# Optimization experiments

Measured on AMD Instinct MI355X. Metric: run time of the kernel, lower is better.

Reference implementation:

```python
import jax, jax.numpy as jnp
import numpy as np

N, E, D, H, C, HID, ED = 50000, 800000, 128, 8, 16, 512, 32


def setup_inputs() -> dict:
    key = jax.random.key(0)
    ks = jax.random.split(key, 16)
    s = 0.05
    return {
        "h": jax.random.normal(ks[0], (N, D), jnp.float32),
        "edge_index": jax.random.randint(ks[1], (2, E), 0, N, jnp.int64),
        "edge_attr": jax.random.normal(ks[2], (E, ED), jnp.float32),
        "w1": jax.random.normal(ks[3], (D, HID), jnp.float32) * s,
        "b1": jnp.zeros((HID,), jnp.float32),
        "w2": jax.random.normal(ks[4], (HID, D), jnp.float32) * s,
        "b2": jnp.zeros((D,), jnp.float32),
        "ln_g": jnp.ones((D,), jnp.float32),
        "ln_b": jnp.zeros((D,), jnp.float32),
        "Wl": jax.random.normal(ks[5], (D, H * C), jnp.float32) * s,
        "bl": jnp.zeros((H * C,), jnp.float32),
        "Wr": jax.random.normal(ks[6], (D, H * C), jnp.float32) * s,
        "br": jnp.zeros((H * C,), jnp.float32),
        "We": jax.random.normal(ks[7], (ED, H * C), jnp.float32) * s,
        "att": jax.random.normal(ks[8], (H, C), jnp.float32) * s,
        "bias_out": jnp.zeros((H * C,), jnp.float32),
    }


def _layer_norm(x, g, b, eps=1e-5):
    mu = jnp.mean(x, axis=-1, keepdims=True)
    var = jnp.var(x, axis=-1, keepdims=True)
    return (x - mu) * jax.lax.rsqrt(var + eps) * g + b


def reference(h, edge_index, edge_attr, w1, b1, w2, b2, ln_g, ln_b,
              Wl, bl, Wr, br, We, att, bias_out):
    # FFN + residual + LayerNorm (dropout = identity in eval)
    u = jax.nn.relu(h @ w1 + b1) @ w2 + b2
    v = _layer_norm(h + u, ln_g, ln_b)

    src, dst = edge_index[0], edge_index[1]
    # GATv2Conv: separate source/target transforms + edge transform
    xl = (v @ Wl + bl).reshape(N, H, C)
    xr = (v @ Wr + br).reshape(N, H, C)
    xe = (edge_attr @ We).reshape(E, H, C)
    x = jax.nn.leaky_relu(xl[src] + xr[dst] + xe, 0.2)  # [E,H,C]
    logits = jnp.einsum("ehc,hc->eh", x, att)            # [E,H]
    # segment softmax over incoming edges of each destination node
    m = jax.lax.stop_gradient(jax.ops.segment_max(logits, dst, num_segments=N))
    ex = jnp.exp(logits - m[dst])
    den = jax.ops.segment_sum(ex, dst, num_segments=N)
    alpha = ex / den[dst]                                # [E,H]
    msg = xl[src] * alpha[..., None]                     # [E,H,C]
    w = jax.ops.segment_sum(msg, dst, num_segments=N).reshape(N, H * C) + bias_out
    output = _layer_norm(w + v, ln_g, ln_b)
    return output, alpha
```

## Files before the change

### kernel.cpp

```cpp
#include <hip/hip_runtime.h>
#include <math.h>

#define N_NODES 50000
#define E_EDGES 800000
#define D_DIM   128
#define H_HEADS 8
#define C_CH    16
#define HID_DIM 512
#define ED_DIM  32

typedef __attribute__((ext_vector_type(8))) short short8;
typedef __attribute__((ext_vector_type(4))) float f32x4;

__device__ __forceinline__ short f2bf(float f) {
    unsigned u = __float_as_uint(f);
    return (short)((u + 0x7FFFu + ((u >> 16) & 1u)) >> 16);
}
__device__ __forceinline__ float bf2f(short s) {
    return __uint_as_float(((unsigned)(unsigned short)s) << 16);
}

__global__ __launch_bounds__(64) void repack_kernel(
    const float* __restrict__ w1, const float* __restrict__ w2,
    const float* __restrict__ Wl, const float* __restrict__ Wr,
    const float* __restrict__ We,
    short8* __restrict__ w1p, short8* __restrict__ w2p,
    short8* __restrict__ Wlp, short8* __restrict__ Wrp,
    short8* __restrict__ Wep)
{
    int b = blockIdx.x;
    const float* src; short8* dst; int Nw, nc, rel;
    if (b < 128)      { src = w1; dst = w1p; Nw = 512; nc = 4;  rel = b; }
    else if (b < 256) { src = w2; dst = w2p; Nw = 128; nc = 16; rel = b - 128; }
    else if (b < 288) { src = Wl; dst = Wlp; Nw = 128; nc = 4;  rel = b - 256; }
    else if (b < 320) { src = Wr; dst = Wrp; Nw = 128; nc = 4;  rel = b - 288; }
    else              { src = We; dst = Wep; Nw = 128; nc = 1;  rel = b - 320; }
    int t = rel / nc, c = rel % nc;
    int l = threadIdx.x, quad = l >> 4, col = l & 15;
    short8 r;
    #pragma unroll
    for (int j = 0; j < 8; ++j)
        r[j] = f2bf(src[(size_t)(c * 32 + quad * 8 + j) * Nw + t * 16 + col]);
    dst[(size_t)rel * 64 + l] = r;
}

__global__ __launch_bounds__(256) void count_kernel(
    const int* __restrict__ edge_index, unsigned* __restrict__ cnt,
    unsigned short* __restrict__ rank)
{
    int e = blockIdx.x * 256 + threadIdx.x;
    int dst = edge_index[E_EDGES + e];
    rank[e] = (unsigned short)atomicAdd(&cnt[dst], 1u);
}

__global__ __launch_bounds__(256) void node_ffn_mfma(
    const float* __restrict__ h,
    const float* __restrict__ b1, const float* __restrict__ b2,
    const float* __restrict__ ln_g, const float* __restrict__ ln_b,
    const float* __restrict__ bl, const float* __restrict__ br,
    const short8* __restrict__ w1p, const short8* __restrict__ w2p,
    const short8* __restrict__ Wlp, const short8* __restrict__ Wrp,
    float* __restrict__ v_out, float* __restrict__ xl_out, float* __restrict__ xr_out)
{
    __shared__ short hid_bf[16 * 520];
    __shared__ float v_s[16 * 132];
    __shared__ short v_bf[16 * 136];

    const int tid = threadIdx.x;
    const int w = tid >> 6, lane = tid & 63;
    const int m = lane & 15, quad = lane >> 4;
    const int n0 = blockIdx.x * 16;

    short8 af[4];
    #pragma unroll
    for (int c = 0; c < 4; ++c) {
        const float* hp = h + (size_t)(n0 + m) * 128 + c * 32 + quad * 8;
        float4 p0 = ((const float4*)hp)[0];
        float4 p1 = ((const float4*)hp)[1];
        short8 a;
        a[0] = f2bf(p0.x); a[1] = f2bf(p0.y); a[2] = f2bf(p0.z); a[3] = f2bf(p0.w);
        a[4] = f2bf(p1.x); a[5] = f2bf(p1.y); a[6] = f2bf(p1.z); a[7] = f2bf(p1.w);
        af[c] = a;
    }

    {
        f32x4 acc[8];
        #pragma unroll
        for (int t = 0; t < 8; ++t) acc[t] = (f32x4){0.f, 0.f, 0.f, 0.f};
        #pragma unroll
        for (int t = 0; t < 8; ++t) {
            int tile = w * 8 + t;
            #pragma unroll
            for (int c = 0; c < 4; ++c) {
                short8 bf = w1p[(size_t)(tile * 4 + c) * 64 + lane];
                acc[t] = __builtin_amdgcn_mfma_f32_16x16x32_bf16(af[c], bf, acc[t], 0, 0, 0);
            }
        }
        #pragma unroll
        for (int t = 0; t < 8; ++t) {
            int col = (w * 8 + t) * 16 + m;
            float bias = b1[col];
            #pragma unroll
            for (int r = 0; r < 4; ++r) {
                int row = quad * 4 + r;
                hid_bf[row * 520 + col] = f2bf(fmaxf(acc[t][r] + bias, 0.f));
            }
        }
    }
    __syncthreads();

    {
        f32x4 acc2[2];
        acc2[0] = (f32x4){0.f, 0.f, 0.f, 0.f};
        acc2[1] = (f32x4){0.f, 0.f, 0.f, 0.f};
        #pragma unroll 4
        for (int c = 0; c < 16; ++c) {
            short8 a = *(const short8*)&hid_bf[m * 520 + c * 32 + quad * 8];
            #pragma unroll
            for (int t = 0; t < 2; ++t) {
                short8 bf = w2p[(size_t)((w * 2 + t) * 16 + c) * 64 + lane];
                acc2[t] = __builtin_amdgcn_mfma_f32_16x16x32_bf16(a, bf, acc2[t], 0, 0, 0);
            }
        }
        #pragma unroll
        for (int t = 0; t < 2; ++t) {
            int col = (w * 2 + t) * 16 + m;
            float bias = b2[col];
            #pragma unroll
            for (int r = 0; r < 4; ++r) {
                int row = quad * 4 + r;
                v_s[row * 132 + col] = acc2[t][r] + bias + h[(size_t)(n0 + row) * 128 + col];
            }
        }
    }
    __syncthreads();

    {
        float g0 = ln_g[lane], g1 = ln_g[lane + 64];
        float be0 = ln_b[lane], be1 = ln_b[lane + 64];
        #pragma unroll
        for (int p = 0; p < 4; ++p) {
            int nd = w * 4 + p;
            float x0 = v_s[nd * 132 + lane], x1 = v_s[nd * 132 + lane + 64];
            float s = x0 + x1, ss = x0 * x0 + x1 * x1;
            #pragma unroll
            for (int off = 1; off < 64; off <<= 1) {
                s  += __shfl_xor(s, off);
                ss += __shfl_xor(ss, off);
            }
            float mu = s * (1.f / 128.f);
            float var = ss * (1.f / 128.f) - mu * mu;
            float rs = rsqrtf(var + 1e-5f);
            float y0 = (x0 - mu) * rs * g0 + be0;
            float y1 = (x1 - mu) * rs * g1 + be1;
            v_out[(size_t)(n0 + nd) * 128 + lane]      = y0;
            v_out[(size_t)(n0 + nd) * 128 + lane + 64] = y1;
            v_bf[nd * 136 + lane]      = f2bf(y0);
            v_bf[nd * 136 + lane + 64] = f2bf(y1);
        }
    }
    __syncthreads();

    {
        short8 af3[4];
        #pragma unroll
        for (int c = 0; c < 4; ++c)
            af3[c] = *(const short8*)&v_bf[m * 136 + c * 32 + quad * 8];
        f32x4 accl[2], accr[2];
        #pragma unroll
        for (int t = 0; t < 2; ++t) {
            accl[t] = (f32x4){0.f, 0.f, 0.f, 0.f};
            accr[t] = (f32x4){0.f, 0.f, 0.f, 0.f};
        }
        #pragma unroll
        for (int t = 0; t < 2; ++t) {
            int tile = w * 2 + t;
            #pragma unroll
            for (int c = 0; c < 4; ++c) {
                accl[t] = __builtin_amdgcn_mfma_f32_16x16x32_bf16(
                    af3[c], Wlp[(size_t)(tile * 4 + c) * 64 + lane], accl[t], 0, 0, 0);
                accr[t] = __builtin_amdgcn_mfma_f32_16x16x32_bf16(
                    af3[c], Wrp[(size_t)(tile * 4 + c) * 64 + lane], accr[t], 0, 0, 0);
            }
        }
        #pragma unroll
        for (int t = 0; t < 2; ++t) {
            int col = (w * 2 + t) * 16 + m;
            float bld = bl[col], brd = br[col];
            #pragma unroll
            for (int r = 0; r < 4; ++r) {
                int row = quad * 4 + r;
                xl_out[(size_t)(n0 + row) * 128 + col] = accl[t][r] + bld;
                xr_out[(size_t)(n0 + row) * 128 + col] = accr[t][r] + brd;
            }
        }
    }
}

__global__ __launch_bounds__(1024) void scan_kernel(
    const unsigned* __restrict__ cnt, int* __restrict__ rowstart)
{
    __shared__ int wsum[16];
    __shared__ int s_carry;
    const int t = threadIdx.x, wv = t >> 6, lane = t & 63;
    if (t == 0) s_carry = 0;
    __syncthreads();
    for (int b4 = 0; b4 < N_NODES / 4; b4 += 1024) {
        int i4 = b4 + t;
        int4 v4 = make_int4(0, 0, 0, 0);
        if (i4 < N_NODES / 4) v4 = ((const int4*)cnt)[i4];
        int v = v4.x + v4.y + v4.z + v4.w;
        int s = v;
        #pragma unroll
        for (int off = 1; off < 64; off <<= 1) {
            int nb = __shfl_up(s, off);
            if (lane >= off) s += nb;
        }
        if (lane == 63) wsum[wv] = s;
        __syncthreads();
        int woff = s_carry;
        for (int k = 0; k < wv; ++k) woff += wsum[k];
        int tot = woff + s;
        if (i4 < N_NODES / 4) {
            int e0 = woff + s - v;
            int4 r;
            r.x = e0;
            r.y = e0 + v4.x;
            r.z = r.y + v4.y;
            r.w = r.z + v4.z;
            ((int4*)rowstart)[i4] = r;
        }
        __syncthreads();
        if (t == 1023) s_carry = tot;
    }
}

__global__ __launch_bounds__(256) void scatter_kernel(
    const int* __restrict__ edge_index, const unsigned short* __restrict__ rank,
    const int* __restrict__ rowstart, int* __restrict__ eidx,
    unsigned* __restrict__ srcdst)
{
    int e = blockIdx.x * 256 + threadIdx.x;
    if (e >= E_EDGES) return;
    int src = edge_index[e];
    int dst = edge_index[E_EDGES + e];
    int pos = rowstart[dst] + (int)rank[e];
    eidx[pos] = e;
    srcdst[pos] = (unsigned)src | ((unsigned)dst << 16);
}

__global__ __launch_bounds__(256) void edge_logits_mfma(
    const int* __restrict__ eidx, const unsigned* __restrict__ srcdst,
    const float* __restrict__ edge_attr,
    const short8* __restrict__ Wep, const float* __restrict__ att,
    const float* __restrict__ xl, const float* __restrict__ xr,
    float* __restrict__ logits_out)
{
    __shared__ short8 We_f[512];
    __shared__ short xe_s[64 * 136];
    __shared__ int e_s[64];
    __shared__ unsigned sd_s[64];
    const int tid = threadIdx.x;
    const int w = tid >> 6, lane = tid & 63;
    const int m = lane & 15, quad = lane >> 4;
    const int p0b = blockIdx.x * 64;

    We_f[tid]       = Wep[tid];
    We_f[tid + 256] = Wep[tid + 256];
    if (tid < 64) {
        int pos = p0b + tid;
        e_s[tid]  = eidx[pos];
        sd_s[tid] = srcdst[pos];
    }
    __syncthreads();

    const float* eap = edge_attr + (size_t)e_s[w * 16 + m] * 32 + quad * 8;
    float4 p0 = ((const float4*)eap)[0];
    float4 p1 = ((const float4*)eap)[1];
    short8 a;
    a[0] = f2bf(p0.x); a[1] = f2bf(p0.y); a[2] = f2bf(p0.z); a[3] = f2bf(p0.w);
    a[4] = f2bf(p1.x); a[5] = f2bf(p1.y); a[6] = f2bf(p1.z); a[7] = f2bf(p1.w);

    f32x4 acc[8];
    #pragma unroll
    for (int t = 0; t < 8; ++t) acc[t] = (f32x4){0.f, 0.f, 0.f, 0.f};
    #pragma unroll
    for (int t = 0; t < 8; ++t)
        acc[t] = __builtin_amdgcn_mfma_f32_16x16x32_bf16(a, We_f[t * 64 + lane], acc[t], 0, 0, 0);

    #pragma unroll
    for (int t = 0; t < 8; ++t) {
        #pragma unroll
        for (int r = 0; r < 4; ++r)
            xe_s[(w * 16 + quad * 4 + r) * 136 + t * 16 + m] = f2bf(acc[t][r]);
    }
    __syncthreads();

    const int g = quad;
    const int s = m;
    const int d0 = s * 8;
    float4 at0 = ((const float4*)(att + d0))[0];
    float4 at1 = ((const float4*)(att + d0))[1];

    #pragma unroll
    for (int p = 0; p < 4; ++p) {
        int el = p * 16 + w * 4 + g;
        unsigned sd = sd_s[el];
        int src = (int)(sd & 0xffffu);
        int dst = (int)(sd >> 16);
        const float4* xlp = (const float4*)(xl + (size_t)src * 128 + d0);
        const float4* xrp = (const float4*)(xr + (size_t)dst * 128 + d0);
        float4 a0 = xlp[0], a1 = xlp[1];
        float4 r0 = xrp[0], r1 = xrp[1];
        short8 xe8 = *(const short8*)&xe_s[el * 136 + d0];

        float xv[8] = { a0.x + r0.x + bf2f(xe8[0]), a0.y + r0.y + bf2f(xe8[1]),
                        a0.z + r0.z + bf2f(xe8[2]), a0.w + r0.w + bf2f(xe8[3]),
                        a1.x + r1.x + bf2f(xe8[4]), a1.y + r1.y + bf2f(xe8[5]),
                        a1.z + r1.z + bf2f(xe8[6]), a1.w + r1.w + bf2f(xe8[7]) };
        float atv[8] = { at0.x, at0.y, at0.z, at0.w, at1.x, at1.y, at1.z, at1.w };
        float pq = 0.f;
        #pragma unroll
        for (int dd = 0; dd < 8; ++dd) {
            float x = xv[dd];
            x = (x > 0.f) ? x : 0.2f * x;
            pq += x * atv[dd];
        }
        pq += __shfl_xor(pq, 1);
        if ((s & 1) == 0) {
            int e = e_s[el];
            logits_out[(size_t)e * 8 + (s >> 1)] = pq;
        }
    }
}

__global__ __launch_bounds__(256) void node_aggregate_kernel(
    const int* __restrict__ eidx, const int* __restrict__ rowstart,
    const unsigned* __restrict__ cnt, const unsigned* __restrict__ srcdst,
    const float* __restrict__ xl, const float* __restrict__ v,
    const float* __restrict__ bias_out,
    const float* __restrict__ ln_g, const float* __restrict__ ln_b,
    float* __restrict__ alphabuf, float* __restrict__ out)
{
    const int wv = threadIdx.x >> 6, lane = threadIdx.x & 63;
    const int n = blockIdx.x * 4 + wv;
    if (n >= N_NODES) return;
    const int start = rowstart[n];
    const int num = (int)cnt[n];

    const int hh = lane & 7;
    const int slot = lane >> 3;

    float den = 0.f;
    for (int i = slot; i < num; i += 8) {
        int e = eidx[start + i];
        den += expf(alphabuf[(size_t)e * 8 + hh]);
    }
    den += __shfl_xor(den, 8);
    den += __shfl_xor(den, 16);
    den += __shfl_xor(den, 32);
    float inv = 1.f / den;

    const int g = lane >> 4, s = lane & 15;
    const int h3 = s >> 1;
    float iv3 = __shfl(inv, h3);
    float acc[8] = {0.f, 0.f, 0.f, 0.f, 0.f, 0.f, 0.f, 0.f};
    for (int i = 0; i < num; i += 4) {
        int ii = i + g;
        if (ii < num) {
            int e = eidx[start + ii];
            int src = (int)(srcdst[start + ii] & 0xffffu);
            float lg = alphabuf[(size_t)e * 8 + h3];
            float al = expf(lg) * iv3;
            if ((s & 1) == 0) alphabuf[(size_t)e * 8 + h3] = al;
            const float4* xp = (const float4*)(xl + (size_t)src * 128 + s * 8);
            float4 q0 = xp[0], q1 = xp[1];
            acc[0] += q0.x * al; acc[1] += q0.y * al;
            acc[2] += q0.z * al; acc[3] += q0.w * al;
            acc[4] += q1.x * al; acc[5] += q1.y * al;
            acc[6] += q1.z * al; acc[7] += q1.w * al;
        }
    }
    #pragma unroll
    for (int k = 0; k < 8; ++k) {
        acc[k] += __shfl_xor(acc[k], 16);
        acc[k] += __shfl_xor(acc[k], 32);
    }

    const float* vp = v + (size_t)n * 128 + s * 8;
    float4 v0 = ((const float4*)vp)[0], v1 = ((const float4*)vp)[1];
    float4 b0 = ((const float4*)(bias_out + s * 8))[0];
    float4 b1 = ((const float4*)(bias_out + s * 8))[1];
    float x[8];
    x[0] = acc[0] + b0.x + v0.x; x[1] = acc[1] + b0.y + v0.y;
    x[2] = acc[2] + b0.z + v0.z; x[3] = acc[3] + b0.w + v0.w;
    x[4] = acc[4] + b1.x + v1.x; x[5] = acc[5] + b1.y + v1.y;
    x[6] = acc[6] + b1.z + v1.z; x[7] = acc[7] + b1.w + v1.w;
    float sm = 0.f, ssm = 0.f;
    #pragma unroll
    for (int k = 0; k < 8; ++k) { sm += x[k]; ssm += x[k] * x[k]; }
    #pragma unroll
    for (int off = 1; off < 16; off <<= 1) {
        sm  += __shfl_xor(sm, off);
        ssm += __shfl_xor(ssm, off);
    }
    float mu = sm * (1.f / 128.f);
    float var = ssm * (1.f / 128.f) - mu * mu;
    float rs = rsqrtf(var + 1e-5f);
    if (g == 0) {
        float4 g0 = ((const float4*)(ln_g + s * 8))[0];
        float4 g1 = ((const float4*)(ln_g + s * 8))[1];
        float4 be0 = ((const float4*)(ln_b + s * 8))[0];
        float4 be1 = ((const float4*)(ln_b + s * 8))[1];
        float4 o0, o1;
        o0.x = (x[0] - mu) * rs * g0.x + be0.x;
        o0.y = (x[1] - mu) * rs * g0.y + be0.y;
        o0.z = (x[2] - mu) * rs * g0.z + be0.z;
        o0.w = (x[3] - mu) * rs * g0.w + be0.w;
        o1.x = (x[4] - mu) * rs * g1.x + be1.x;
        o1.y = (x[5] - mu) * rs * g1.y + be1.y;
        o1.z = (x[6] - mu) * rs * g1.z + be1.z;
        o1.w = (x[7] - mu) * rs * g1.w + be1.w;
        float4* op = (float4*)(out + (size_t)n * 128 + s * 8);
        op[0] = o0; op[1] = o1;
    }
}

extern "C" void kernel_launch(void* const* d_in, const int* in_sizes, int n_in,
                              void* d_out, int out_size, void* d_ws, size_t ws_size,
                              hipStream_t stream)
{
    const float* h        = (const float*)d_in[0];
    const int*   edge_idx = (const int*)  d_in[1];
    const float* edge_attr= (const float*)d_in[2];
    const float* w1       = (const float*)d_in[3];
    const float* b1       = (const float*)d_in[4];
    const float* w2       = (const float*)d_in[5];
    const float* b2       = (const float*)d_in[6];
    const float* ln_g     = (const float*)d_in[7];
    const float* ln_b     = (const float*)d_in[8];
    const float* Wl       = (const float*)d_in[9];
    const float* bl       = (const float*)d_in[10];
    const float* Wr       = (const float*)d_in[11];
    const float* br       = (const float*)d_in[12];
    const float* We       = (const float*)d_in[13];
    const float* att      = (const float*)d_in[14];
    const float* bias_out = (const float*)d_in[15];

    float* out   = (float*)d_out;
    float* alpha = out + (size_t)N_NODES * 128;

    short8* w1p = (short8*)alpha;
    short8* w2p = w1p + 128 * 64;
    short8* Wlp = w2p + 128 * 64;
    short8* Wrp = Wlp + 32 * 64;

    float*          v        = (float*)d_ws;
    float*          xl       = v  + (size_t)N_NODES * 128;
    float*          xr       = xl + (size_t)N_NODES * 128;
    unsigned*       cnt      = (unsigned*)(xr + (size_t)N_NODES * 128);
    int*            rowstart = (int*)(cnt + N_NODES);
    unsigned short* rank     = (unsigned short*)(rowstart + N_NODES);
    short8*         Wep      = (short8*)(rank + E_EDGES);
    int*            eidx     = (int*)(Wep + 512);
    unsigned*       srcdst   = (unsigned*)(eidx + E_EDGES);

    hipMemsetAsync(cnt, 0, (size_t)N_NODES * sizeof(unsigned), stream);

    repack_kernel<<<328, 64, 0, stream>>>(w1, w2, Wl, Wr, We,
                                          w1p, w2p, Wlp, Wrp, Wep);
    count_kernel<<<E_EDGES / 256, 256, 0, stream>>>(edge_idx, cnt, rank);
    node_ffn_mfma<<<N_NODES / 16, 256, 0, stream>>>(
        h, b1, b2, ln_g, ln_b, bl, br, w1p, w2p, Wlp, Wrp, v, xl, xr);
    scan_kernel<<<1, 1024, 0, stream>>>(cnt, rowstart);
    scatter_kernel<<<(E_EDGES + 255) / 256, 256, 0, stream>>>(
        edge_idx, rank, rowstart, eidx, srcdst);
    edge_logits_mfma<<<E_EDGES / 64, 256, 0, stream>>>(
        eidx, srcdst, edge_attr, Wep, att, xl, xr, alpha);
    node_aggregate_kernel<<<(N_NODES + 3) / 4, 256, 0, stream>>>(
        eidx, rowstart, cnt, srcdst, xl, v, bias_out, ln_g, ln_b, alpha, out);
}
```

Before: 496.6 us.

## Store xl/xr in bf16 and keep logits in CSR order

The node FFN kernel now writes the xl and xr projections as bf16 instead of fp32. This halves the bytes of the random per-edge gathers in the logits and aggregation kernels. Logits are also written to a CSR-ordered scratch buffer, so the aggregation kernel reads them contiguously instead of through the eidx indirection; only the final alpha is scattered to edge order. The cost is extra bf16 rounding on xl/xr, which affects accuracy, and a separate E×8 logits buffer in the workspace.

```diff
diff --git a/kernel.cpp b/kernel.cpp
--- a/kernel.cpp
+++ b/kernel.cpp
@@ -60,7 +60,8 @@
     const float* __restrict__ bl, const float* __restrict__ br,
     const short8* __restrict__ w1p, const short8* __restrict__ w2p,
     const short8* __restrict__ Wlp, const short8* __restrict__ Wrp,
-    float* __restrict__ v_out, float* __restrict__ xl_out, float* __restrict__ xr_out)
+    float* __restrict__ v_out,
+    unsigned short* __restrict__ xl_bf_out, unsigned short* __restrict__ xr_bf_out)
 {
     __shared__ short hid_bf[16 * 520];
     __shared__ float v_s[16 * 132];
@@ -190,8 +191,8 @@
             #pragma unroll
             for (int r = 0; r < 4; ++r) {
                 int row = quad * 4 + r;
-                xl_out[(size_t)(n0 + row) * 128 + col] = accl[t][r] + bld;
-                xr_out[(size_t)(n0 + row) * 128 + col] = accr[t][r] + brd;
+                xl_bf_out[(size_t)(n0 + row) * 128 + col] = (unsigned short)f2bf(accl[t][r] + bld);
+                xr_bf_out[(size_t)(n0 + row) * 128 + col] = (unsigned short)f2bf(accr[t][r] + brd);
             }
         }
     }
@@ -253,8 +254,8 @@
     const int* __restrict__ eidx, const unsigned* __restrict__ srcdst,
     const float* __restrict__ edge_attr,
     const short8* __restrict__ Wep, const float* __restrict__ att,
-    const float* __restrict__ xl, const float* __restrict__ xr,
-    float* __restrict__ logits_out)
+    const unsigned short* __restrict__ xl_bf, const unsigned short* __restrict__ xr_bf,
+    float* __restrict__ logits_csr)
 {
     __shared__ short8 We_f[512];
     __shared__ short xe_s[64 * 136];
@@ -308,39 +309,32 @@
         unsigned sd = sd_s[el];
         int src = (int)(sd & 0xffffu);
         int dst = (int)(sd >> 16);
-        const float4* xlp = (const float4*)(xl + (size_t)src * 128 + d0);
-        const float4* xrp = (const float4*)(xr + (size_t)dst * 128 + d0);
-        float4 a0 = xlp[0], a1 = xlp[1];
-        float4 r0 = xrp[0], r1 = xrp[1];
+        short8 xl8 = *(const short8*)&xl_bf[(size_t)src * 128 + d0];
+        short8 xr8 = *(const short8*)&xr_bf[(size_t)dst * 128 + d0];
         short8 xe8 = *(const short8*)&xe_s[el * 136 + d0];
 
-        float xv[8] = { a0.x + r0.x + bf2f(xe8[0]), a0.y + r0.y + bf2f(xe8[1]),
-                        a0.z + r0.z + bf2f(xe8[2]), a0.w + r0.w + bf2f(xe8[3]),
-                        a1.x + r1.x + bf2f(xe8[4]), a1.y + r1.y + bf2f(xe8[5]),
-                        a1.z + r1.z + bf2f(xe8[6]), a1.w + r1.w + bf2f(xe8[7]) };
         float atv[8] = { at0.x, at0.y, at0.z, at0.w, at1.x, at1.y, at1.z, at1.w };
         float pq = 0.f;
         #pragma unroll
         for (int dd = 0; dd < 8; ++dd) {
-            float x = xv[dd];
+            float x = bf2f(xl8[dd]) + bf2f(xr8[dd]) + bf2f(xe8[dd]);
             x = (x > 0.f) ? x : 0.2f * x;
             pq += x * atv[dd];
         }
         pq += __shfl_xor(pq, 1);
-        if ((s & 1) == 0) {
-            int e = e_s[el];
-            logits_out[(size_t)e * 8 + (s >> 1)] = pq;
-        }
+        if ((s & 1) == 0)
+            logits_csr[(size_t)(p0b + el) * 8 + (s >> 1)] = pq;
     }
 }
 
 __global__ __launch_bounds__(256) void node_aggregate_kernel(
     const int* __restrict__ eidx, const int* __restrict__ rowstart,
     const unsigned* __restrict__ cnt, const unsigned* __restrict__ srcdst,
-    const float* __restrict__ xl, const float* __restrict__ v,
+    const float* __restrict__ logits_csr,
+    const unsigned short* __restrict__ xl_bf, const float* __restrict__ v,
     const float* __restrict__ bias_out,
     const float* __restrict__ ln_g, const float* __restrict__ ln_b,
-    float* __restrict__ alphabuf, float* __restrict__ out)
+    float* __restrict__ alpha_out, float* __restrict__ out)
 {
     const int wv = threadIdx.x >> 6, lane = threadIdx.x & 63;
     const int n = blockIdx.x * 4 + wv;
@@ -353,8 +347,7 @@
 
     float den = 0.f;
     for (int i = slot; i < num; i += 8) {
-        int e = eidx[start + i];
-        den += expf(alphabuf[(size_t)e * 8 + hh]);
+        den += expf(logits_csr[(size_t)(start + i) * 8 + hh]);
     }
     den += __shfl_xor(den, 8);
     den += __shfl_xor(den, 16);
@@ -370,15 +363,14 @@
         if (ii < num) {
             int e = eidx[start + ii];
             int src = (int)(srcdst[start + ii] & 0xffffu);
-            float lg = alphabuf[(size_t)e * 8 + h3];
+            float lg = logits_csr[(size_t)(start + ii) * 8 + h3];
             float al = expf(lg) * iv3;
-            if ((s & 1) == 0) alphabuf[(size_t)e * 8 + h3] = al;
-            const float4* xp = (const float4*)(xl + (size_t)src * 128 + s * 8);
-            float4 q0 = xp[0], q1 = xp[1];
-            acc[0] += q0.x * al; acc[1] += q0.y * al;
-            acc[2] += q0.z * al; acc[3] += q0.w * al;
-            acc[4] += q1.x * al; acc[5] += q1.y * al;
-            acc[6] += q1.z * al; acc[7] += q1.w * al;
+            if ((s & 1) == 0) alpha_out[(size_t)e * 8 + h3] = al;
+            short8 q = *(const short8*)&xl_bf[(size_t)src * 128 + s * 8];
+            acc[0] += bf2f(q[0]) * al; acc[1] += bf2f(q[1]) * al;
+            acc[2] += bf2f(q[2]) * al; acc[3] += bf2f(q[3]) * al;
+            acc[4] += bf2f(q[4]) * al; acc[5] += bf2f(q[5]) * al;
+            acc[6] += bf2f(q[6]) * al; acc[7] += bf2f(q[7]) * al;
         }
     }
     #pragma unroll
@@ -456,9 +448,10 @@
     short8* Wrp = Wlp + 32 * 64;
 
     float*          v        = (float*)d_ws;
-    float*          xl       = v  + (size_t)N_NODES * 128;
-    float*          xr       = xl + (size_t)N_NODES * 128;
-    unsigned*       cnt      = (unsigned*)(xr + (size_t)N_NODES * 128);
+    unsigned short* xl_bf    = (unsigned short*)(v + (size_t)N_NODES*128);
+    unsigned short* xr_bf    = xl_bf + (size_t)N_NODES * 128;
+    float*          lcsr     = (float*)(xr_bf + (size_t)N_NODES * 128);
+    unsigned*       cnt      = (unsigned*)(lcsr + (size_t)E_EDGES * 8);
     int*            rowstart = (int*)(cnt + N_NODES);
     unsigned short* rank     = (unsigned short*)(rowstart + N_NODES);
     short8*         Wep      = (short8*)(rank + E_EDGES);
@@ -471,12 +464,12 @@
                                           w1p, w2p, Wlp, Wrp, Wep);
     count_kernel<<<E_EDGES / 256, 256, 0, stream>>>(edge_idx, cnt, rank);
     node_ffn_mfma<<<N_NODES / 16, 256, 0, stream>>>(
-        h, b1, b2, ln_g, ln_b, bl, br, w1p, w2p, Wlp, Wrp, v, xl, xr);
+        h, b1, b2, ln_g, ln_b, bl, br, w1p, w2p, Wlp, Wrp, v, xl_bf, xr_bf);
     scan_kernel<<<1, 1024, 0, stream>>>(cnt, rowstart);
     scatter_kernel<<<(E_EDGES + 255) / 256, 256, 0, stream>>>(
         edge_idx, rank, rowstart, eidx, srcdst);
     edge_logits_mfma<<<E_EDGES / 64, 256, 0, stream>>>(
-        eidx, srcdst, edge_attr, Wep, att, xl, xr, alpha);
+        eidx, srcdst, edge_attr, Wep, att, xl_bf, xr_bf, lcsr);
     node_aggregate_kernel<<<(N_NODES + 3) / 4, 256, 0, stream>>>(
-        eidx, rowstart, cnt, srcdst, xl, v, bias_out, ln_g, ln_b, alpha, out);
-}
+        eidx, rowstart, cnt, srcdst, lcsr, xl_bf, v, bias_out, ln_g, ln_b, alpha, out);
+}
```

Measured after the change: 452.8 us. -8.8%, faster.
